# Kernel tuning notes

Measured on AMD Instinct MI355X. Metric: run time of the kernel, lower is better.

Reference implementation:

```python
import jax, jax.numpy as jnp
import numpy as np

NE = 14          # NUM_ELEMENTS
NC = 20          # NUM_CHANNEL
DEN = NE         # density channel
GRV = NE + 1     # gravity channel

# (id, density, gravity) per element, in id order
_ELEMS = [(0,1,1),(1,4,0),(2,3,1),(3,2,1),(4,0,1),(5,4,0),(6,4,0),(7,0,1),(8,4,0),(9,3,1),(10,3,1),(11,2,1),(12,3,1),(13,4,0)]

def _elem_table():
    t = np.zeros((NE, NC), dtype=np.float32)
    for eid, dens, grav in _ELEMS:
        t[eid, eid] = 1.0
        t[eid, DEN] = dens
        t[eid, GRV] = grav
    return jnp.asarray(t)

# torch.roll semantics: get_above(x)[h] = x[h-1] (wrap)
above = lambda x: jnp.roll(x, 1, axis=2)
below = lambda x: jnp.roll(x, -1, axis=2)
left  = lambda x: jnp.roll(x, 1, axis=3)
right = lambda x: jnp.roll(x, -1, axis=3)

def interp2(sa, sb, if_false, if_a, if_b):
    # faithful to torch: (~a & ~b)*f + a*xa + b*xb (bools broadcast-multiply floats)
    return (jnp.logical_and(~sa, ~sb)) * if_false + sa * if_a + sb * if_b

def setup_inputs() -> dict:
    key = jax.random.key(0)
    k1, k2 = jax.random.split(key)
    B, H, W = 8, 512, 512
    ids = jax.random.randint(k1, (B, H, W), 0, NE)
    world = _elem_table()[ids]                 # [B,H,W,NC]
    world = jnp.transpose(world, (0, 3, 1, 2)) # [B,NC,H,W]
    rand_movement = jax.random.uniform(k2, (B, 1, H, W), dtype=jnp.float32)
    return {"world": world, "rand_movement": rand_movement}

def reference(world, rand_movement):
    B, C, H, W = world.shape
    # --- stone support check (conv2d with zero padding, taps at top-left/top-right) ---
    stone = world[:, 9:10]
    p = jnp.pad(stone, ((0, 0), (0, 0), (1, 1), (1, 1)))
    supports = p[:, :, 0:H, 0:W] + p[:, :, 0:H, 2:W + 2]  # stone[h-1,w-1]+stone[h-1,w+1]
    new_grav = (1.0 - stone) * world[:, GRV:GRV + 1] + stone * (supports < 2)
    world = world.at[:, GRV:GRV + 1].set(new_grav)

    # --- vertical gravity passes over densities 0..3 ---
    did_gravity = jnp.zeros((B, 1, H, W), dtype=world.dtype)
    for curr_density in (0, 1, 2, 3):
        density = world[:, DEN:DEN + 1]
        is_density_above_greater = (above(density) - density) > 0
        is_density_below_less = below(is_density_above_greater)
        is_density_current = density == curr_density
        is_density_above_current = above(is_density_current)
        is_gravity = world[:, GRV:GRV + 1] == 1
        is_cb_gravity = jnp.logical_and(below(is_gravity), is_gravity)
        is_ca_gravity = jnp.logical_and(above(is_gravity), is_gravity)
        does_become_below = is_density_current & is_density_below_less & is_cb_gravity
        does_become_above = is_density_above_greater & is_density_above_current & is_ca_gravity
        did_gravity = did_gravity + does_become_above
        world = interp2(does_become_below, does_become_above, world, below(world), above(world))

    # --- diagonal fall for sand (2) and dust (12) ---
    for elem in (2, 12):
        fall_dir = rand_movement > 0.5
        not_did_gravity = did_gravity <= 0
        for fall_left in (True, False):
            g_dir = left if fall_left else right
            g_not = right if fall_left else left
            is_element = world[:, elem:elem + 1] == 1
            is_ar_element = g_not(above(is_element))
            density = world[:, DEN:DEN + 1]
            is_matching_fall = fall_dir if fall_left else ~fall_dir
            is_ar_matching_fall = g_not(above(is_matching_fall))
            is_bl_density_lower = (density - g_dir(below(density))) > 0
            is_ar_density_higher = (g_not(above(density)) - density) > 0
            is_gravity = world[:, GRV:GRV + 1] == 1
            is_bl_gravity = jnp.logical_and(g_dir(below(is_gravity)), is_gravity)
            is_ar_gravity = jnp.logical_and(g_not(above(is_gravity)), is_gravity)
            ndg_bl = jnp.logical_and(g_dir(below(not_did_gravity)), not_did_gravity)
            ndg_ar = jnp.logical_and(g_not(above(not_did_gravity)), not_did_gravity)
            does_become_bl = is_element & ndg_bl & is_matching_fall & is_bl_density_lower & is_bl_gravity
            does_become_ar = is_ar_element & ndg_ar & is_ar_matching_fall & is_ar_density_higher & is_ar_gravity
            world = interp2(does_become_bl, does_become_ar, world, g_dir(below(world)), g_not(above(world)))
    return world
```

## Files before the change

### kernel.cpp

```cpp
#include <hip/hip_runtime.h>
#include <stdint.h>

#define HH 512
#define WW 512
#define PLANE (HH*WW)
#define NCH 20

#define GRAV_PACK 0x1E9Du

__device__ __forceinline__ uint32_t eqz4(uint32_t x) {
    uint32_t nz = (x | (x >> 1) | (x >> 2) | (x >> 3)) & 0x01010101u;
    return nz ^ 0x01010101u;
}
__device__ __forceinline__ uint32_t gtb(uint32_t a, uint32_t b) {
    uint32_t t = (a | 0x08080808u) - b;
    return ((t + 0x07070707u) & 0x10101010u) >> 4;
}
__device__ __forceinline__ uint32_t bmask(uint32_t b) {
    uint32_t h = b << 7;
    return (h - (h >> 7)) | h;
}

__device__ __forceinline__ uint32_t pack_cell(float d_,
                                              float c1_, float c5_, float c6_, float c8_,
                                              float c2_, float c9_, float c10_,
                                              float c3_, float c4_) {
    int d = (int)d_;
    int e;
    if (d == 4)      e = (c1_ != 0.f) ? 1 : (c5_ != 0.f) ? 5 : (c6_ != 0.f) ? 6 : (c8_ != 0.f) ? 8 : 13;
    else if (d == 3) e = (c2_ != 0.f) ? 2 : (c9_ != 0.f) ? 9 : (c10_ != 0.f) ? 10 : 12;
    else if (d == 2) e = (c3_ != 0.f) ? 3 : 11;
    else if (d == 1) e = 0;
    else             e = (c4_ != 0.f) ? 4 : 7;
    int g = (int)((GRAV_PACK >> e) & 1u);
    return (uint32_t)(e | (g << 4) | (d << 5));
}

__global__ __launch_bounds__(256) void extract_k(const float* __restrict__ world,
                                                 uint32_t* __restrict__ st) {
    int idx = blockIdx.x * 256 + threadIdx.x;
    int b  = idx >> 16;
    int p4 = idx & 0xFFFF;
    const float4* base = (const float4*)(world + (size_t)b * NCH * PLANE) + p4;
    float4 vD  = base[14 * (PLANE / 4)];
    float4 v1  = base[ 1 * (PLANE / 4)];
    float4 v5  = base[ 5 * (PLANE / 4)];
    float4 v6  = base[ 6 * (PLANE / 4)];
    float4 v8  = base[ 8 * (PLANE / 4)];
    float4 v2  = base[ 2 * (PLANE / 4)];
    float4 v9  = base[ 9 * (PLANE / 4)];
    float4 v10 = base[10 * (PLANE / 4)];
    float4 v3  = base[ 3 * (PLANE / 4)];
    float4 v4  = base[ 4 * (PLANE / 4)];
    uint32_t b0 = pack_cell(vD.x, v1.x, v5.x, v6.x, v8.x, v2.x, v9.x, v10.x, v3.x, v4.x);
    uint32_t b1 = pack_cell(vD.y, v1.y, v5.y, v6.y, v8.y, v2.y, v9.y, v10.y, v3.y, v4.y);
    uint32_t b2 = pack_cell(vD.z, v1.z, v5.z, v6.z, v8.z, v2.z, v9.z, v10.z, v3.z, v4.z);
    uint32_t b3 = pack_cell(vD.w, v1.w, v5.w, v6.w, v8.w, v2.w, v9.w, v10.w, v3.w, v4.w);
    st[idx] = b0 | (b1 << 8) | (b2 << 16) | (b3 << 24);
}

#define TILE_R 32
#define TILE_C 64
#define HALO_T 9
#define HALO_B 8
#define HALO_W 8
#define RH (TILE_R + HALO_T + HALO_B)
#define RWW 20
#define RWS 21
#define NW (RH*RWW)
#define NOWN 4

__global__ __launch_bounds__(256, 2) void sim_k(const uint8_t* __restrict__ st_in,
                                                const float* __restrict__ rnd,
                                                float* __restrict__ out) {
    __shared__ uint32_t bufA[RH * RWS];
    __shared__ uint32_t bufB[RH * RWS];
    __shared__ uint32_t aux [RH * RWS];

    const int tid = threadIdx.x;
    const int h0  = blockIdx.y * TILE_R;
    const int w0  = blockIdx.x * TILE_C;

    uint32_t sreg[NOWN], freg[NOWN], dgreg[NOWN];

    auto zero4 = [&](float* ob) {
        float4 z = {0.f, 0.f, 0.f, 0.f};
        for (int idx = tid; idx < 4 * TILE_R * 16; idx += 256) {
            int cw = idx & 15, row = (idx >> 4) & (TILE_R - 1), c = 16 + (idx >> 9);
            *(float4*)(ob + (size_t)c * PLANE + (size_t)(h0 + row) * WW + (w0 + cw * 4)) = z;
        }
    };

    auto stage = [&](const uint8_t* stb, const float* rb) {
#pragma unroll
        for (int k = 0; k < NOWN; ++k) {
            int r = tid + k * 256;
            if (r < NW) {
                int i = r / RWW, jw = r - i * RWW;
                int gh  = (h0 + i - HALO_T) & (HH - 1);
                int gwb = (w0 + jw * 4 - HALO_W) & (WW - 1);
                uint32_t w = *(const uint32_t*)(stb + gh * WW + gwb);
                bufA[i * RWS + jw] = w;
                sreg[k] = w;
                float4 rv = *(const float4*)(rb + gh * WW + gwb);
                uint32_t aw = 0;
                aw |= (rv.x > 0.5f) ? 0x00000001u : 0u;
                aw |= (rv.y > 0.5f) ? 0x00000100u : 0u;
                aw |= (rv.z > 0.5f) ? 0x00010000u : 0u;
                aw |= (rv.w > 0.5f) ? 0x01000000u : 0u;
                freg[k] = aw;
                dgreg[k] = 0u;
            }
        }
    };

    auto passes = [&]() {
#pragma unroll
        for (int k = 0; k < NOWN; ++k) {
            int r = tid + k * 256;
            if (r < NW) {
                int i = r / RWW, jw = r - i * RWW;
                uint32_t s = sreg[k];
                uint32_t stm = eqz4((s & 0x0F0F0F0Fu) ^ 0x09090909u);
                int im = (i > 0) ? i - 1 : 0;
                int jl = (jw > 0) ? jw - 1 : 0;
                int jr = (jw < RWW - 1) ? jw + 1 : RWW - 1;
                uint32_t wU  = bufA[im * RWS + jw];
                uint32_t wUL = bufA[im * RWS + jl];
                uint32_t wUR = bufA[im * RWS + jr];
                uint32_t upL = (wU << 8) | (wUL >> 24);
                uint32_t upR = (wU >> 8) | (wUR << 24);
                uint32_t stL = eqz4((upL & 0x0F0F0F0Fu) ^ 0x09090909u);
                uint32_t stR = eqz4((upR & 0x0F0F0F0Fu) ^ 0x09090909u);
                int gh  = (h0 + i - HALO_T) & (HH - 1);
                int gwb = (w0 + jw * 4 - HALO_W) & (WW - 1);
                uint32_t rowOK = (gh != 0) ? 0x01010101u : 0u;
                uint32_t okL = 0x01010101u ^ ((gwb == 0)      ? 0x00000001u : 0u);
                uint32_t okR = 0x01010101u ^ ((gwb == WW - 4) ? 0x01000000u : 0u);
                uint32_t supL = stL & okL & rowOK;
                uint32_t supR = stR & okR & rowOK;
                uint32_t g2 = 0x01010101u ^ (supL & supR);
                uint32_t ns = (s & ~0x10101010u) | (g2 << 4);
                uint32_t res = s ^ ((s ^ ns) & bmask(stm));
                bufB[i * RWS + jw] = res;
                sreg[k] = res;
            }
        }
        __syncthreads();

        uint32_t* cur = bufB;
        uint32_t* nxt = bufA;

        for (int curr = 0; curr < 4; ++curr) {
            const uint32_t crep = (uint32_t)curr * 0x01010101u;
#pragma unroll
            for (int k = 0; k < NOWN; ++k) {
                int r = tid + k * 256;
                if (r < NW) {
                    int i = r / RWW, jw = r - i * RWW;
                    int ia = (i > 0) ? i - 1 : 0;
                    int ib = (i < RH - 1) ? i + 1 : RH - 1;
                    uint32_t s  = sreg[k];
                    uint32_t sa = cur[ia * RWS + jw];
                    uint32_t sb = cur[ib * RWS + jw];
                    uint32_t d  = (s  >> 5) & 0x07070707u;
                    uint32_t da = (sa >> 5) & 0x07070707u;
                    uint32_t db = (sb >> 5) & 0x07070707u;
                    uint32_t g  = (s  >> 4) & 0x01010101u;
                    uint32_t ga = (sa >> 4) & 0x01010101u;
                    uint32_t gb = (sb >> 4) & 0x01010101u;
                    uint32_t bel = eqz4(d ^ crep)  & gtb(d, db) & gb & g;
                    uint32_t abv = eqz4(da ^ crep) & gtb(da, d) & ga & g;
                    uint32_t res = s ^ ((s ^ sb) & bmask(bel)) ^ ((s ^ sa) & bmask(abv));
                    nxt[i * RWS + jw] = res;
                    sreg[k] = res;
                    dgreg[k] |= abv;
                    if (curr == 3)
                        aux[i * RWS + jw] = freg[k] | (dgreg[k] << 1);
                }
            }
            __syncthreads();
            uint32_t* t = cur; cur = nxt; nxt = t;
        }

        for (int pass = 0; pass < 4; ++pass) {
            const int  elem = (pass < 2) ? 2 : 12;
            const bool fl   = ((pass & 1) == 0);
            const uint32_t erep = (uint32_t)elem * 0x01010101u;
#pragma unroll
            for (int k = 0; k < NOWN; ++k) {
                int r = tid + k * 256;
                if (r < NW) {
                    int i = r / RWW, jw = r - i * RWW;
                    int ia = (i > 0) ? i - 1 : 0;
                    int ib = (i < RH - 1) ? i + 1 : RH - 1;
                    int jl = (jw > 0) ? jw - 1 : 0;
                    int jr = (jw < RWW - 1) ? jw + 1 : RWW - 1;
                    uint32_t s  = sreg[k];
                    uint32_t wB = cur[ib * RWS + jw];
                    uint32_t wA = cur[ia * RWS + jw];
                    uint32_t aB = aux[ib * RWS + jw];
                    uint32_t aA = aux[ia * RWS + jw];
                    uint32_t sbl, sar, abl, aar;
                    if (fl) {
                        uint32_t wBL = cur[ib * RWS + jl], wAR = cur[ia * RWS + jr];
                        uint32_t aBL = aux[ib * RWS + jl], aAR = aux[ia * RWS + jr];
                        sbl = (wB << 8) | (wBL >> 24);
                        sar = (wA >> 8) | (wAR << 24);
                        abl = (aB << 8) | (aBL >> 24);
                        aar = (aA >> 8) | (aAR << 24);
                    } else {
                        uint32_t wBR = cur[ib * RWS + jr], wAL = cur[ia * RWS + jl];
                        uint32_t aBR = aux[ib * RWS + jr], aAL = aux[ia * RWS + jl];
                        sbl = (wB >> 8) | (wBR << 24);
                        sar = (wA << 8) | (wAL >> 24);
                        abl = (aB >> 8) | (aBR << 24);
                        aar = (aA << 8) | (aAL >> 24);
                    }
                    uint32_t d   = (s   >> 5) & 0x07070707u;
                    uint32_t dbl = (sbl >> 5) & 0x07070707u;
                    uint32_t dar = (sar >> 5) & 0x07070707u;
                    uint32_t g   = (s   >> 4) & 0x01010101u;
                    uint32_t gbl = (sbl >> 4) & 0x01010101u;
                    uint32_t gar = (sar >> 4) & 0x01010101u;
                    uint32_t ndg   = dgreg[k] ^ 0x01010101u;
                    uint32_t ndgbl = ((~abl) >> 1) & 0x01010101u;
                    uint32_t ndgar = ((~aar) >> 1) & 0x01010101u;
                    uint32_t mtc = (fl ? freg[k] : ~freg[k]) & 0x01010101u;
                    uint32_t mta = (fl ? aar : ~aar) & 0x01010101u;
                    uint32_t eqe  = eqz4((s   & 0x0F0F0F0Fu) ^ erep);
                    uint32_t eqer = eqz4((sar & 0x0F0F0F0Fu) ^ erep);
                    uint32_t bbl = eqe  & ndgbl & ndg & mtc & gtb(d, dbl) & gbl & g;
                    uint32_t bar = eqer & ndgar & ndg & mta & gtb(dar, d) & gar & g;
                    uint32_t res = s ^ ((s ^ sbl) & bmask(bbl)) ^ ((s ^ sar) & bmask(bar));
                    nxt[i * RWS + jw] = res;
                    sreg[k] = res;
                }
            }
            __syncthreads();
            uint32_t* t = cur; cur = nxt; nxt = t;
        }
    };

    auto expand = [&](float* ob) {
#pragma unroll
        for (int k = 0; k < 2; ++k) {
            int ci  = tid + k * 256;
            int row = ci >> 4, cw = ci & 15;
            uint32_t w = bufB[(HALO_T + row) * RWS + (HALO_W / 4) + cw];
            float* base = ob + (size_t)(h0 + row) * WW + (w0 + cw * 4);
#pragma unroll
            for (int c = 0; c < 16; ++c) {
                float4 v;
                float* vv = &v.x;
#pragma unroll
                for (int q = 0; q < 4; ++q) {
                    uint32_t byte = (w >> (8 * q)) & 0xFFu;
                    float val;
                    if (c < 14)       val = ((byte & 15u) == (uint32_t)c) ? 1.0f : 0.0f;
                    else if (c == 14) val = (float)((byte >> 5) & 7u);
                    else              val = (float)((byte >> 4) & 1u);
                    vv[q] = val;
                }
                *(float4*)(base + (size_t)c * PLANE) = v;
            }
        }
    };

    const int bA = blockIdx.z, bB = blockIdx.z + 4;
    const uint8_t* stA = st_in + (size_t)bA * PLANE;
    const uint8_t* stB = st_in + (size_t)bB * PLANE;
    const float*   rA  = rnd   + (size_t)bA * PLANE;
    const float*   rB  = rnd   + (size_t)bB * PLANE;
    float* obA = out + (size_t)bA * NCH * PLANE;
    float* obB = out + (size_t)bB * NCH * PLANE;

    zero4(obA);
    stage(stA, rA);
    __syncthreads();
    passes();

    zero4(obB);
    stage(stB, rB);
    expand(obA);
    __syncthreads();
    passes();
    expand(obB);
}

extern "C" void kernel_launch(void* const* d_in, const int* in_sizes, int n_in,
                              void* d_out, int out_size, void* d_ws, size_t ws_size,
                              hipStream_t stream) {
    const float* world = (const float*)d_in[0];
    const float* rnd   = (const float*)d_in[1];
    float* out = (float*)d_out;
    uint32_t* st = (uint32_t*)d_ws;

    extract_k<<<2048, 256, 0, stream>>>(world, st);

    dim3 grid(WW / TILE_C, HH / TILE_R, 4);
    sim_k<<<grid, 256, 0, stream>>>((const uint8_t*)st, rnd, out);
}
```

Before: 58.36 us.

## Interleave first batch's output stores with second batch's simulation passes

The separate zero-fill and expand phases are removed. The first batch's 20 output channels are now written two at a time inside each of the ten synchronised phases of the second batch's simulation, with each thread holding its two packed words in registers. A third shared buffer keeps the first result from being overwritten, and the pass loops are fully unrolled. The aim is to spread the heavy global store traffic across the compute phases instead of leaving it as serial bursts, at the cost of more shared memory and register pressure.

```diff
diff --git a/kernel.cpp b/kernel.cpp
--- a/kernel.cpp
+++ b/kernel.cpp
@@ -70,11 +70,28 @@
 #define NW (RH*RWW)
 #define NOWN 4
 
+__device__ __forceinline__ float4 ch_vals(uint32_t w, int c) {
+    float4 v;
+    float* vv = &v.x;
+#pragma unroll
+    for (int q = 0; q < 4; ++q) {
+        uint32_t byte = (w >> (8 * q)) & 0xFFu;
+        float val;
+        if (c < 14)       val = ((byte & 15u) == (uint32_t)c) ? 1.0f : 0.0f;
+        else if (c == 14) val = (float)((byte >> 5) & 7u);
+        else if (c == 15) val = (float)((byte >> 4) & 1u);
+        else              val = 0.0f;
+        vv[q] = val;
+    }
+    return v;
+}
+
 __global__ __launch_bounds__(256, 2) void sim_k(const uint8_t* __restrict__ st_in,
                                                 const float* __restrict__ rnd,
                                                 float* __restrict__ out) {
     __shared__ uint32_t bufA[RH * RWS];
     __shared__ uint32_t bufB[RH * RWS];
+    __shared__ uint32_t bufC[RH * RWS];
     __shared__ uint32_t aux [RH * RWS];
 
     const int tid = threadIdx.x;
@@ -82,14 +99,8 @@
     const int w0  = blockIdx.x * TILE_C;
 
     uint32_t sreg[NOWN], freg[NOWN], dgreg[NOWN];
-
-    auto zero4 = [&](float* ob) {
-        float4 z = {0.f, 0.f, 0.f, 0.f};
-        for (int idx = tid; idx < 4 * TILE_R * 16; idx += 256) {
-            int cw = idx & 15, row = (idx >> 4) & (TILE_R - 1), c = 16 + (idx >> 9);
-            *(float4*)(ob + (size_t)c * PLANE + (size_t)(h0 + row) * WW + (w0 + cw * 4)) = z;
-        }
-    };
+    uint32_t xw0 = 0, xw1 = 0;
+    float*   xob = nullptr;
 
     auto stage = [&](const uint8_t* stb, const float* rb) {
 #pragma unroll
@@ -114,7 +125,23 @@
         }
     };
 
-    auto passes = [&]() {
+    auto slice = [&](int p) {
+        if (!xob) return;
+#pragma unroll
+        for (int k = 0; k < 2; ++k) {
+            int ci  = tid + k * 256;
+            int row = ci >> 4, cw = ci & 15;
+            uint32_t w = k ? xw1 : xw0;
+            float* base = xob + (size_t)(h0 + row) * WW + (w0 + cw * 4);
+            *(float4*)(base + (size_t)(2 * p)     * PLANE) = ch_vals(w, 2 * p);
+            *(float4*)(base + (size_t)(2 * p + 1) * PLANE) = ch_vals(w, 2 * p + 1);
+        }
+    };
+
+    auto passes = [&](uint32_t* t1, uint32_t* t2) {
+        slice(0);
+        __syncthreads();
+
 #pragma unroll
         for (int k = 0; k < NOWN; ++k) {
             int r = tid + k * 256;
@@ -142,15 +169,17 @@
                 uint32_t g2 = 0x01010101u ^ (supL & supR);
                 uint32_t ns = (s & ~0x10101010u) | (g2 << 4);
                 uint32_t res = s ^ ((s ^ ns) & bmask(stm));
-                bufB[i * RWS + jw] = res;
+                t1[i * RWS + jw] = res;
                 sreg[k] = res;
             }
         }
+        slice(1);
         __syncthreads();
 
-        uint32_t* cur = bufB;
-        uint32_t* nxt = bufA;
-
+        uint32_t* cur = t1;
+        uint32_t* nxt = t2;
+
+#pragma unroll
         for (int curr = 0; curr < 4; ++curr) {
             const uint32_t crep = (uint32_t)curr * 0x01010101u;
 #pragma unroll
@@ -179,10 +208,12 @@
                         aux[i * RWS + jw] = freg[k] | (dgreg[k] << 1);
                 }
             }
+            slice(2 + curr);
             __syncthreads();
             uint32_t* t = cur; cur = nxt; nxt = t;
         }
 
+#pragma unroll
         for (int pass = 0; pass < 4; ++pass) {
             const int  elem = (pass < 2) ? 2 : 12;
             const bool fl   = ((pass & 1) == 0);
@@ -237,33 +268,9 @@
                     sreg[k] = res;
                 }
             }
+            slice(6 + pass);
             __syncthreads();
             uint32_t* t = cur; cur = nxt; nxt = t;
-        }
-    };
-
-    auto expand = [&](float* ob) {
-#pragma unroll
-        for (int k = 0; k < 2; ++k) {
-            int ci  = tid + k * 256;
-            int row = ci >> 4, cw = ci & 15;
-            uint32_t w = bufB[(HALO_T + row) * RWS + (HALO_W / 4) + cw];
-            float* base = ob + (size_t)(h0 + row) * WW + (w0 + cw * 4);
-#pragma unroll
-            for (int c = 0; c < 16; ++c) {
-                float4 v;
-                float* vv = &v.x;
-#pragma unroll
-                for (int q = 0; q < 4; ++q) {
-                    uint32_t byte = (w >> (8 * q)) & 0xFFu;
-                    float val;
-                    if (c < 14)       val = ((byte & 15u) == (uint32_t)c) ? 1.0f : 0.0f;
-                    else if (c == 14) val = (float)((byte >> 5) & 7u);
-                    else              val = (float)((byte >> 4) & 1u);
-                    vv[q] = val;
-                }
-                *(float4*)(base + (size_t)c * PLANE) = v;
-            }
         }
     };
 
@@ -275,17 +282,32 @@
     float* obA = out + (size_t)bA * NCH * PLANE;
     float* obB = out + (size_t)bB * NCH * PLANE;
 
-    zero4(obA);
     stage(stA, rA);
-    __syncthreads();
-    passes();
-
-    zero4(obB);
+    xob = nullptr;
+    passes(bufB, bufA);
+
+    {
+        int row0 = tid >> 4, cw0 = tid & 15;
+        int ci1 = tid + 256;
+        int row1 = ci1 >> 4, cw1 = ci1 & 15;
+        xw0 = bufB[(HALO_T + row0) * RWS + (HALO_W / 4) + cw0];
+        xw1 = bufB[(HALO_T + row1) * RWS + (HALO_W / 4) + cw1];
+        xob = obA;
+    }
+
     stage(stB, rB);
-    expand(obA);
-    __syncthreads();
-    passes();
-    expand(obB);
+    passes(bufC, bufA);
+
+#pragma unroll
+    for (int k = 0; k < 2; ++k) {
+        int ci  = tid + k * 256;
+        int row = ci >> 4, cw = ci & 15;
+        uint32_t w = bufC[(HALO_T + row) * RWS + (HALO_W / 4) + cw];
+        float* base = obB + (size_t)(h0 + row) * WW + (w0 + cw * 4);
+#pragma unroll
+        for (int c = 0; c < NCH; ++c)
+            *(float4*)(base + (size_t)c * PLANE) = ch_vals(w, c);
+    }
 }
 
 extern "C" void kernel_launch(void* const* d_in, const int* in_sizes, int n_in,
```

New measurement: 59.26 us. No clear change (+1.5%).

## Use 512-thread blocks, simplify density compares, and merge zero stores into expand

Applied to the files above, without the earlier changes.

Doubles the block size to 512 threads, so each thread owns 2 tile words instead of 4 and the output expansion maps one thread per core word. The generic byte-wise greater-than helper is replaced by compare-against-constant forms that exploit the known current density or the fixed density bound. The zero-fill of the trailing channels moves into the expand loop, and the expand encoding uses a one-hot shift. The pass loops are unrolled. This trades register count per thread for more threads per block, and relies on the density-range assumptions in the rewritten compares.

```diff
diff --git a/kernel.cpp b/kernel.cpp
--- a/kernel.cpp
+++ b/kernel.cpp
@@ -11,10 +11,6 @@
 __device__ __forceinline__ uint32_t eqz4(uint32_t x) {
     uint32_t nz = (x | (x >> 1) | (x >> 2) | (x >> 3)) & 0x01010101u;
     return nz ^ 0x01010101u;
-}
-__device__ __forceinline__ uint32_t gtb(uint32_t a, uint32_t b) {
-    uint32_t t = (a | 0x08080808u) - b;
-    return ((t + 0x07070707u) & 0x10101010u) >> 4;
 }
 __device__ __forceinline__ uint32_t bmask(uint32_t b) {
     uint32_t h = b << 7;
@@ -68,11 +64,12 @@
 #define RWW 20
 #define RWS 21
 #define NW (RH*RWW)
-#define NOWN 4
-
-__global__ __launch_bounds__(256, 2) void sim_k(const uint8_t* __restrict__ st_in,
-                                                const float* __restrict__ rnd,
-                                                float* __restrict__ out) {
+#define NT 512
+#define NOWN 2
+
+__global__ __launch_bounds__(NT, 4) void sim_k(const uint8_t* __restrict__ st_in,
+                                               const float* __restrict__ rnd,
+                                               float* __restrict__ out) {
     __shared__ uint32_t bufA[RH * RWS];
     __shared__ uint32_t bufB[RH * RWS];
     __shared__ uint32_t aux [RH * RWS];
@@ -83,18 +80,10 @@
 
     uint32_t sreg[NOWN], freg[NOWN], dgreg[NOWN];
 
-    auto zero4 = [&](float* ob) {
-        float4 z = {0.f, 0.f, 0.f, 0.f};
-        for (int idx = tid; idx < 4 * TILE_R * 16; idx += 256) {
-            int cw = idx & 15, row = (idx >> 4) & (TILE_R - 1), c = 16 + (idx >> 9);
-            *(float4*)(ob + (size_t)c * PLANE + (size_t)(h0 + row) * WW + (w0 + cw * 4)) = z;
-        }
-    };
-
     auto stage = [&](const uint8_t* stb, const float* rb) {
 #pragma unroll
         for (int k = 0; k < NOWN; ++k) {
-            int r = tid + k * 256;
+            int r = tid + k * NT;
             if (r < NW) {
                 int i = r / RWW, jw = r - i * RWW;
                 int gh  = (h0 + i - HALO_T) & (HH - 1);
@@ -117,7 +106,7 @@
     auto passes = [&]() {
 #pragma unroll
         for (int k = 0; k < NOWN; ++k) {
-            int r = tid + k * 256;
+            int r = tid + k * NT;
             if (r < NW) {
                 int i = r / RWW, jw = r - i * RWW;
                 uint32_t s = sreg[k];
@@ -151,11 +140,13 @@
         uint32_t* cur = bufB;
         uint32_t* nxt = bufA;
 
+#pragma unroll
         for (int curr = 0; curr < 4; ++curr) {
             const uint32_t crep = (uint32_t)curr * 0x01010101u;
+            const uint32_t CKP7 = crep + 0x0F0F0F0Fu;
 #pragma unroll
             for (int k = 0; k < NOWN; ++k) {
-                int r = tid + k * 256;
+                int r = tid + k * NT;
                 if (r < NW) {
                     int i = r / RWW, jw = r - i * RWW;
                     int ia = (i > 0) ? i - 1 : 0;
@@ -169,8 +160,8 @@
                     uint32_t g  = (s  >> 4) & 0x01010101u;
                     uint32_t ga = (sa >> 4) & 0x01010101u;
                     uint32_t gb = (sb >> 4) & 0x01010101u;
-                    uint32_t bel = eqz4(d ^ crep)  & gtb(d, db) & gb & g;
-                    uint32_t abv = eqz4(da ^ crep) & gtb(da, d) & ga & g;
+                    uint32_t bel = eqz4(d ^ crep)  & (((CKP7 - db) & 0x10101010u) >> 4) & gb & g;
+                    uint32_t abv = eqz4(da ^ crep) & (((CKP7 - d)  & 0x10101010u) >> 4) & ga & g;
                     uint32_t res = s ^ ((s ^ sb) & bmask(bel)) ^ ((s ^ sa) & bmask(abv));
                     nxt[i * RWS + jw] = res;
                     sreg[k] = res;
@@ -183,13 +174,14 @@
             uint32_t* t = cur; cur = nxt; nxt = t;
         }
 
+#pragma unroll
         for (int pass = 0; pass < 4; ++pass) {
             const int  elem = (pass < 2) ? 2 : 12;
             const bool fl   = ((pass & 1) == 0);
             const uint32_t erep = (uint32_t)elem * 0x01010101u;
 #pragma unroll
             for (int k = 0; k < NOWN; ++k) {
-                int r = tid + k * 256;
+                int r = tid + k * NT;
                 if (r < NW) {
                     int i = r / RWW, jw = r - i * RWW;
                     int ia = (i > 0) ? i - 1 : 0;
@@ -230,8 +222,8 @@
                     uint32_t mta = (fl ? aar : ~aar) & 0x01010101u;
                     uint32_t eqe  = eqz4((s   & 0x0F0F0F0Fu) ^ erep);
                     uint32_t eqer = eqz4((sar & 0x0F0F0F0Fu) ^ erep);
-                    uint32_t bbl = eqe  & ndgbl & ndg & mtc & gtb(d, dbl) & gbl & g;
-                    uint32_t bar = eqer & ndgar & ndg & mta & gtb(dar, d) & gar & g;
+                    uint32_t bbl = eqe  & ndgbl & ndg & mtc & (((0x12121212u - dbl) & 0x10101010u) >> 4) & gbl & g;
+                    uint32_t bar = eqer & ndgar & ndg & mta & (((0x12121212u - d)   & 0x10101010u) >> 4) & gar & g;
                     uint32_t res = s ^ ((s ^ sbl) & bmask(bbl)) ^ ((s ^ sar) & bmask(bar));
                     nxt[i * RWS + jw] = res;
                     sreg[k] = res;
@@ -242,29 +234,31 @@
         }
     };
 
-    auto expand = [&](float* ob) {
-#pragma unroll
-        for (int k = 0; k < 2; ++k) {
-            int ci  = tid + k * 256;
-            int row = ci >> 4, cw = ci & 15;
-            uint32_t w = bufB[(HALO_T + row) * RWS + (HALO_W / 4) + cw];
-            float* base = ob + (size_t)(h0 + row) * WW + (w0 + cw * 4);
-#pragma unroll
-            for (int c = 0; c < 16; ++c) {
-                float4 v;
-                float* vv = &v.x;
-#pragma unroll
-                for (int q = 0; q < 4; ++q) {
-                    uint32_t byte = (w >> (8 * q)) & 0xFFu;
-                    float val;
-                    if (c < 14)       val = ((byte & 15u) == (uint32_t)c) ? 1.0f : 0.0f;
-                    else if (c == 14) val = (float)((byte >> 5) & 7u);
-                    else              val = (float)((byte >> 4) & 1u);
-                    vv[q] = val;
-                }
-                *(float4*)(base + (size_t)c * PLANE) = v;
-            }
-        }
+    auto expand = [&](float* ob, uint32_t w) {
+        float* base = ob + (size_t)(h0 + (tid >> 4)) * WW + (w0 + (tid & 15) * 4);
+        uint32_t oh0 = 1u << ( w        & 15u);
+        uint32_t oh1 = 1u << ((w >>  8) & 15u);
+        uint32_t oh2 = 1u << ((w >> 16) & 15u);
+        uint32_t oh3 = 1u << ((w >> 24) & 15u);
+#pragma unroll
+        for (int c = 0; c < 14; ++c) {
+            float4 v;
+            v.x = (float)((oh0 >> c) & 1u);
+            v.y = (float)((oh1 >> c) & 1u);
+            v.z = (float)((oh2 >> c) & 1u);
+            v.w = (float)((oh3 >> c) & 1u);
+            *(float4*)(base + (size_t)c * PLANE) = v;
+        }
+        float4 vd = { (float)((w >>  5) & 7u), (float)((w >> 13) & 7u),
+                      (float)((w >> 21) & 7u), (float)((w >> 29) & 7u) };
+        *(float4*)(base + (size_t)14 * PLANE) = vd;
+        float4 vg = { (float)((w >>  4) & 1u), (float)((w >> 12) & 1u),
+                      (float)((w >> 20) & 1u), (float)((w >> 28) & 1u) };
+        *(float4*)(base + (size_t)15 * PLANE) = vg;
+        float4 z = {0.f, 0.f, 0.f, 0.f};
+#pragma unroll
+        for (int c = 16; c < 20; ++c)
+            *(float4*)(base + (size_t)c * PLANE) = z;
     };
 
     const int bA = blockIdx.z, bB = blockIdx.z + 4;
@@ -275,17 +269,19 @@
     float* obA = out + (size_t)bA * NCH * PLANE;
     float* obB = out + (size_t)bB * NCH * PLANE;
 
-    zero4(obA);
+    const int coreIdx = (HALO_T + (tid >> 4)) * RWS + (HALO_W / 4) + (tid & 15);
+
     stage(stA, rA);
     __syncthreads();
     passes();
 
-    zero4(obB);
+    uint32_t wA = bufB[coreIdx];
     stage(stB, rB);
-    expand(obA);
+    expand(obA, wA);
     __syncthreads();
     passes();
-    expand(obB);
+
+    expand(obB, bufB[coreIdx]);
 }
 
 extern "C" void kernel_launch(void* const* d_in, const int* in_sizes, int n_in,
@@ -299,5 +295,5 @@
     extract_k<<<2048, 256, 0, stream>>>(world, st);
 
     dim3 grid(WW / TILE_C, HH / TILE_R, 4);
-    sim_k<<<grid, 256, 0, stream>>>((const uint8_t*)st, rnd, out);
-}
+    sim_k<<<grid, NT, 0, stream>>>((const uint8_t*)st, rnd, out);
+}
```

New measurement: 55.60 us. -4.7%, faster.
